# Kernel tuning notes

Measured on AMD Instinct MI355X. Metric: run time of the kernel, lower is better.

## Reference

```python
import jax, jax.numpy as jnp
import numpy as np

KNOTS = 16
BN_EPS = 1e-5  # flax BatchNorm default


def _normalize_spline_params(W, H, D):
    # widths/heights sum to 1 over the [0,1] hypercube; slopes positive
    dx = jax.nn.softmax(W, axis=-1)          # (N, d, K) bin widths
    dy = jax.nn.softmax(H, axis=-1)          # (N, d, K) bin heights
    sl = jax.nn.softplus(D)                  # (N, d, K-1) interior knot slopes
    return dx, dy, sl


def _gather_bin(a, idx):
    # a: (N, d, K'), idx: (N, d) -> (N, d)
    return jnp.take_along_axis(a, idx[..., None], axis=-1)[..., 0]


def _rqs_forward(t, dx, dy, sl):
    """Rational-quadratic spline on [0,1] (Durkan et al. 2019); identity outside.
    t: (N, d); dx, dy: (N, d, K); sl: (N, d, K-1).
    Returns y: (N, d), log_det: (N,)."""
    K = dx.shape[-1]
    zero = jnp.zeros_like(dx[..., :1])
    one = jnp.ones_like(dx[..., :1])
    xk = jnp.concatenate([zero, jnp.cumsum(dx, axis=-1)], axis=-1)   # (N, d, K+1) knot x
    yk = jnp.concatenate([zero, jnp.cumsum(dy, axis=-1)], axis=-1)   # (N, d, K+1) knot y
    dk = jnp.concatenate([one, sl, one], axis=-1)                    # (N, d, K+1) knot slopes

    in_bounds = (t >= 0.0) & (t <= 1.0)
    tc = jnp.clip(t, 0.0, 1.0)
    # per-element bin search (vectorized searchsorted)
    idx = jnp.clip(jnp.sum((tc[..., None] >= xk).astype(jnp.int32), axis=-1) - 1, 0, K - 1)

    xk_b = _gather_bin(xk, idx)
    yk_b = _gather_bin(yk, idx)
    dx_b = _gather_bin(dx, idx)
    dy_b = _gather_bin(dy, idx)
    d0 = _gather_bin(dk, idx)
    d1 = _gather_bin(dk, idx + 1)

    xi = (tc - xk_b) / dx_b            # position within bin, in [0,1]
    s = dy_b / dx_b                    # bin mean slope
    xi1m = xi * (1.0 - xi)
    den = s + (d0 + d1 - 2.0 * s) * xi1m
    y_in = yk_b + dy_b * (s * xi * xi + d0 * xi1m) / den
    dydx = s * s * (d1 * xi * xi + 2.0 * s * xi1m + d0 * (1.0 - xi) ** 2) / (den * den)

    y = jnp.where(in_bounds, y_in, t)
    log_det = jnp.sum(jnp.where(in_bounds, jnp.log(dydx), 0.0), axis=1)  # (N,)
    return y, log_det


def setup_inputs() -> dict:
    key = jax.random.key(0)
    ks = jax.random.split(key, 8)
    N, D, C = 65536, 64, 16
    d = D // 2
    spline_dim = 3 * KNOTS - 1
    cin = d + C           # conditioner input width: hstack(xc, c)
    H1, H2 = 128, 128     # layers=(128,128)

    def dense(k, fi, fo):
        return (jax.random.normal(k, (fi, fo), jnp.float32) / np.float32(np.sqrt(fi)))

    return {
        "x": jax.random.uniform(ks[0], (N, D), jnp.float32),
        "c": jax.random.normal(ks[1], (N, C), jnp.float32),
        "bn_scale": jnp.ones((cin,), jnp.float32),
        "bn_bias": jnp.zeros((cin,), jnp.float32),
        "bn_mean": 0.1 * jax.random.normal(ks[2], (cin,), jnp.float32),
        "bn_var": jax.random.uniform(ks[3], (cin,), jnp.float32, minval=0.5, maxval=1.5),
        "W0": dense(ks[4], cin, H1), "b0": jnp.zeros((H1,), jnp.float32),
        "W1": dense(ks[5], H1, H2), "b1": jnp.zeros((H2,), jnp.float32),
        "W2": dense(ks[6], H2, d * spline_dim), "b2": jnp.zeros((d * spline_dim,), jnp.float32),
    }


def reference(x, c, bn_scale, bn_bias, bn_mean, bn_var, W0, b0, W1, b1, W2, b2):
    N, D = x.shape
    d = D // 2
    xt, xc = x[:, :d], x[:, d:]
    h = jnp.hstack((xc, c))
    # BatchNorm in eval mode (use_running_average=True)
    h = (h - bn_mean) * jax.lax.rsqrt(bn_var + BN_EPS) * bn_scale + bn_bias
    h = jax.nn.swish(h @ W0 + b0)
    h = jax.nn.swish(h @ W1 + b1)
    p = (h @ W2 + b2).reshape(N, d, 3 * KNOTS - 1)
    dx, dy, sl = _normalize_spline_params(
        p[..., :KNOTS], p[..., KNOTS:2 * KNOTS], p[..., 2 * KNOTS:])
    yt, log_det = _rqs_forward(xt, dx, dy, sl)
    y = jnp.hstack((yt, xc))
    return y, log_det
```

## Files before the change

kernel.cpp:

```cpp
#include <hip/hip_runtime.h>
#include <math.h>

#define BN_EPS 1e-5f
#define ROWS 64

typedef __attribute__((ext_vector_type(8))) short short8;
typedef __attribute__((ext_vector_type(4))) float float4v;

__device__ __forceinline__ unsigned short f2bf(float f) {
    union { float f; unsigned int u; } v; v.f = f;
    unsigned int r = v.u + 0x7FFF + ((v.u >> 16) & 1);
    return (unsigned short)(r >> 16);
}
__device__ __forceinline__ float softplus_f(float v) {
    float e = __expf(-fabsf(v));
    float r = __logf(1.f + e);
    return v > 0.f ? v + r : r;
}
__device__ __forceinline__ float swish_f(float a) {
    return a / (1.f + __expf(-a));
}

#define PREP_WIDE_THREADS (1536 * 128 + 128 * 128)
__global__ void prep_weights(const float* __restrict__ W0, const float* __restrict__ W1,
                             const float* __restrict__ W2, const float* __restrict__ b0,
                             const float* __restrict__ b2,
                             const float* __restrict__ bn_scale, const float* __restrict__ bn_bias,
                             const float* __restrict__ bn_mean, const float* __restrict__ bn_var,
                             unsigned short* __restrict__ Wt0, unsigned short* __restrict__ Wt1,
                             unsigned short* __restrict__ Wt2, float* __restrict__ b0p,
                             float* __restrict__ b2p) {
    const int bid = blockIdx.x, tid = threadIdx.x;
    if (bid < 832) {
        int i = bid * 256 + tid;
        if (i < 1536 * 128) {
            int k = i / 1536, colp = i - k * 1536;
            int dd = colp / 48, j = colp - dd * 48;
            float v = (j < 47) ? W2[k * 1504 + dd * 47 + j] : 0.f;
            Wt2[(size_t)colp * 128 + k] = f2bf(v);
        } else {
            int i2 = i - 1536 * 128;
            int k = i2 >> 7, n = i2 & 127;
            Wt1[n * 128 + k] = f2bf(W1[k * 128 + n]);
        }
        return;
    }
    if (bid == 832) {
        __shared__ float lds[48 * 129 + 96];
        float* a   = lds + 48 * 129;
        float* bsh = a + 48;
        if (tid < 48) {
            float av = bn_scale[tid] * rsqrtf(bn_var[tid] + BN_EPS);
            a[tid] = av;
            bsh[tid] = bn_bias[tid] - bn_mean[tid] * av;
        }
        for (int idx = tid; idx < 48 * 128; idx += 256) {
            int k = idx >> 7, n = idx & 127;
            lds[k * 129 + n] = W0[k * 128 + n];
        }
        __syncthreads();
        #pragma unroll 4
        for (int it = 0; it < 32; ++it) {
            int n = (tid >> 6) + it * 4;
            int k = tid & 63;
            float v = (k < 48) ? lds[k * 129 + n] * a[k] : 0.f;
            Wt0[n * 64 + k] = f2bf(v);
        }
        if (tid < 128) {
            float s = b0[tid];
            #pragma unroll
            for (int k = 0; k < 48; ++k) s += bsh[k] * lds[k * 129 + tid];
            b0p[tid] = s;
        }
        return;
    }
    for (int e = tid; e < 32 * 48; e += 256) {
        int dd = e / 48, j = e - dd * 48;
        b2p[e] = (j < 47) ? b2[dd * 47 + j] : 0.f;
    }
}

__launch_bounds__(256, 4)
__global__ void nsc_mfma(const float* __restrict__ x, const float* __restrict__ c,
                         const unsigned short* __restrict__ Wt0, const float* __restrict__ b0p,
                         const unsigned short* __restrict__ Wt1, const float* __restrict__ b1,
                         const unsigned short* __restrict__ Wt2, const float* __restrict__ b2p,
                         float* __restrict__ out, int N) {
    __shared__ __align__(16) char smem[38912];
    unsigned short* h0 = (unsigned short*)smem;
    unsigned short* h2 = (unsigned short*)smem;
    unsigned short* h1 = (unsigned short*)(smem + 17408);
    float*          ldp = (float*)(smem + 17408 + 20480);

    const int tid  = threadIdx.x;
    const int lane = tid & 63;
    const int l    = lane & 15;
    const int q    = lane >> 4;
    const int wu   = __builtin_amdgcn_readfirstlane(tid >> 6);
    const int r0   = blockIdx.x * ROWS;
    float* pw = (float*)(smem + 17408) + wu * (64 * 20);

    for (int idx = tid; idx < 64 * 64; idx += 256) {
        int r = idx >> 6, j = idx & 63;
        float h = 0.f;
        if (j < 48) {
            int row = r0 + r;
            h = (j < 32) ? x[(size_t)row * 64 + 32 + j] : c[(size_t)row * 16 + (j - 32)];
        }
        h0[r * 72 + j] = f2bf(h);
    }
    for (int idx = tid; idx < 64 * 8; idx += 256) {
        int r = idx >> 3, ch = idx & 7;
        float4v v = *(const float4v*)(x + (size_t)(r0 + r) * 64 + 32 + ch * 4);
        *(float4v*)(out + (size_t)(r0 + r) * 64 + 32 + ch * 4) = v;
    }
    __syncthreads();

    {
        float4v acc[2][4];
        float4v z = {0.f, 0.f, 0.f, 0.f};
        #pragma unroll
        for (int nt = 0; nt < 2; ++nt)
            #pragma unroll
            for (int mt = 0; mt < 4; ++mt) acc[nt][mt] = z;
        #pragma unroll
        for (int ks = 0; ks < 2; ++ks) {
            short8 a[4];
            #pragma unroll
            for (int mt = 0; mt < 4; ++mt)
                a[mt] = *(const short8*)(h0 + (mt * 16 + l) * 72 + ks * 32 + (q << 3));
            #pragma unroll
            for (int nt = 0; nt < 2; ++nt) {
                int n0 = (wu * 2 + nt) * 16;
                short8 b = *(const short8*)(Wt0 + (n0 + l) * 64 + ks * 32 + (q << 3));
                #pragma unroll
                for (int mt = 0; mt < 4; ++mt)
                    acc[nt][mt] = __builtin_amdgcn_mfma_f32_16x16x32_bf16(a[mt], b, acc[nt][mt], 0, 0, 0);
            }
        }
        #pragma unroll
        for (int nt = 0; nt < 2; ++nt) {
            int n0 = (wu * 2 + nt) * 16;
            float bb = b0p[n0 + l];
            #pragma unroll
            for (int mt = 0; mt < 4; ++mt)
                #pragma unroll
                for (int r = 0; r < 4; ++r)
                    h1[(mt * 16 + q * 4 + r) * 136 + n0 + l] = f2bf(swish_f(acc[nt][mt][r] + bb));
        }
    }
    __syncthreads();

    {
        float4v acc[2][4];
        float4v z = {0.f, 0.f, 0.f, 0.f};
        #pragma unroll
        for (int nt = 0; nt < 2; ++nt)
            #pragma unroll
            for (int mt = 0; mt < 4; ++mt) acc[nt][mt] = z;
        #pragma unroll
        for (int ks = 0; ks < 4; ++ks) {
            short8 a[4];
            #pragma unroll
            for (int mt = 0; mt < 4; ++mt)
                a[mt] = *(const short8*)(h1 + (mt * 16 + l) * 136 + ks * 32 + (q << 3));
            #pragma unroll
            for (int nt = 0; nt < 2; ++nt) {
                int n0 = (wu * 2 + nt) * 16;
                short8 b = *(const short8*)(Wt1 + (n0 + l) * 128 + ks * 32 + (q << 3));
                #pragma unroll
                for (int mt = 0; mt < 4; ++mt)
                    acc[nt][mt] = __builtin_amdgcn_mfma_f32_16x16x32_bf16(a[mt], b, acc[nt][mt], 0, 0, 0);
            }
        }
        #pragma unroll
        for (int nt = 0; nt < 2; ++nt) {
            int n0 = (wu * 2 + nt) * 16;
            float bb = b1[n0 + l];
            #pragma unroll
            for (int mt = 0; mt < 4; ++mt)
                #pragma unroll
                for (int r = 0; r < 4; ++r)
                    h2[(mt * 16 + q * 4 + r) * 136 + n0 + l] = f2bf(swish_f(acc[nt][mt][r] + bb));
        }
    }
    __syncthreads();

    float ld_local = 0.f;
    float yreg[8];
    for (int pass = 0; pass < 8; ++pass) {
        const int d = wu * 8 + pass;
        float t = x[(size_t)(r0 + lane) * 64 + d];
        bool inb = (t >= 0.f) && (t <= 1.f);
        float tc = fminf(fmaxf(t, 0.f), 1.f);

        float4v acc[3][4];
        float4v z = {0.f, 0.f, 0.f, 0.f};
        #pragma unroll
        for (int jt = 0; jt < 3; ++jt)
            #pragma unroll
            for (int smt = 0; smt < 4; ++smt) acc[jt][smt] = z;
        #pragma unroll
        for (int ks = 0; ks < 4; ++ks) {
            short8 bf[4];
            #pragma unroll
            for (int smt = 0; smt < 4; ++smt)
                bf[smt] = *(const short8*)(h2 + (smt * 16 + l) * 136 + ks * 32 + (q << 3));
            #pragma unroll
            for (int jt = 0; jt < 3; ++jt) {
                short8 a = *(const short8*)(Wt2 + (size_t)(d * 48 + jt * 16 + l) * 128 + ks * 32 + (q << 3));
                #pragma unroll
                for (int smt = 0; smt < 4; ++smt)
                    acc[jt][smt] = __builtin_amdgcn_mfma_f32_16x16x32_bf16(a, bf[smt], acc[jt][smt], 0, 0, 0);
            }
        }

        float pr[16];
        {
            float4v bj = *(const float4v*)(b2p + d * 48 + (q << 2));
            #pragma unroll
            for (int smt = 0; smt < 4; ++smt)
                *(float4v*)(pw + (smt * 16 + l) * 20 + (q << 2)) = acc[0][smt] + bj;
            #pragma unroll
            for (int c2 = 0; c2 < 4; ++c2)
                *(float4v*)(pr + c2 * 4) = *(const float4v*)(pw + lane * 20 + c2 * 4);
        }
        float mW = pr[0];
        #pragma unroll
        for (int i = 1; i < 16; ++i) mW = fmaxf(mW, pr[i]);
        float sW = 0.f;
        #pragma unroll
        for (int i = 0; i < 16; ++i) { pr[i] = __expf(pr[i] - mW); sW += pr[i]; }
        float invW = 1.f / sW;
        float cum = 0.f, xkb = 0.f, dxb = pr[0] * invW;
        int idx = 0;
        #pragma unroll
        for (int i = 0; i < 16; ++i) {
            float dxi = pr[i] * invW;
            bool cnd = (tc >= cum);
            idx = cnd ? i   : idx;
            xkb = cnd ? cum : xkb;
            dxb = cnd ? dxi : dxb;
            cum += dxi;
        }

        {
            float4v bj = *(const float4v*)(b2p + d * 48 + 16 + (q << 2));
            #pragma unroll
            for (int smt = 0; smt < 4; ++smt)
                *(float4v*)(pw + (smt * 16 + l) * 20 + (q << 2)) = acc[1][smt] + bj;
            #pragma unroll
            for (int c2 = 0; c2 < 4; ++c2)
                *(float4v*)(pr + c2 * 4) = *(const float4v*)(pw + lane * 20 + c2 * 4);
        }
        float mH = pr[0];
        #pragma unroll
        for (int i = 1; i < 16; ++i) mH = fmaxf(mH, pr[i]);
        float sH = 0.f;
        #pragma unroll
        for (int i = 0; i < 16; ++i) { pr[i] = __expf(pr[i] - mH); sH += pr[i]; }
        float invH = 1.f / sH;
        float ykb = 0.f, dyb = pr[0] * invH;
        #pragma unroll
        for (int i = 0; i < 16; ++i) {
            float dyi = pr[i] * invH;
            ykb += (i < idx) ? dyi : 0.f;
            dyb  = (i == idx) ? dyi : dyb;
        }

        {
            float4v bj = *(const float4v*)(b2p + d * 48 + 32 + (q << 2));
            #pragma unroll
            for (int smt = 0; smt < 4; ++smt)
                *(float4v*)(pw + (smt * 16 + l) * 20 + (q << 2)) = acc[2][smt] + bj;
        }
        int i0 = (idx > 0)  ? idx - 1 : 0;
        int i1 = (idx < 15) ? idx     : 14;
        float pa0 = pw[lane * 20 + i0];
        float pa1 = pw[lane * 20 + i1];
        float d0 = (idx == 0)  ? 1.f : softplus_f(pa0);
        float d1 = (idx == 15) ? 1.f : softplus_f(pa1);

        float xi  = (tc - xkb) / dxb;
        float s   = dyb / dxb;
        float xim = 1.f - xi;
        float x1m = xi * xim;
        float den = s + (d0 + d1 - 2.f * s) * x1m;
        float y_in = ykb + dyb * (s * xi * xi + d0 * x1m) / den;
        float dydx = s * s * (d1 * xi * xi + 2.f * s * x1m + d0 * xim * xim) / (den * den);

        yreg[pass] = inb ? y_in : t;
        ld_local += inb ? __logf(dydx) : 0.f;
    }

    {
        float4v* o = (float4v*)(out + (size_t)(r0 + lane) * 64 + wu * 8);
        o[0] = *(const float4v*)(yreg);
        o[1] = *(const float4v*)(yreg + 4);
    }
    ldp[wu * 64 + lane] = ld_local;
    __syncthreads();
    if (tid < 64) {
        out[(size_t)N * 64 + r0 + tid] =
            ldp[tid] + ldp[64 + tid] + ldp[128 + tid] + ldp[192 + tid];
    }
}

extern "C" void kernel_launch(void* const* d_in, const int* in_sizes, int n_in,
                              void* d_out, int out_size, void* d_ws, size_t ws_size,
                              hipStream_t stream) {
    const float* x        = (const float*)d_in[0];
    const float* c        = (const float*)d_in[1];
    const float* bn_scale = (const float*)d_in[2];
    const float* bn_bias  = (const float*)d_in[3];
    const float* bn_mean  = (const float*)d_in[4];
    const float* bn_var   = (const float*)d_in[5];
    const float* W0       = (const float*)d_in[6];
    const float* b0       = (const float*)d_in[7];
    const float* W1       = (const float*)d_in[8];
    const float* b1       = (const float*)d_in[9];
    const float* W2       = (const float*)d_in[10];
    const float* b2       = (const float*)d_in[11];
    float* out = (float*)d_out;

    unsigned short* Wt0 = (unsigned short*)d_ws;
    unsigned short* Wt1 = Wt0 + 128 * 64;
    unsigned short* Wt2 = Wt1 + 128 * 128;
    float*          b2p = (float*)(Wt2 + 1536 * 128);
    float*          b0p = b2p + 32 * 48;

    const int N = in_sizes[0] / 64;
    prep_weights<<<834, 256, 0, stream>>>(W0, W1, W2, b0, b2,
                                          bn_scale, bn_bias, bn_mean, bn_var,
                                          Wt0, Wt1, Wt2, b0p, b2p);
    nsc_mfma<<<N / ROWS, 256, 0, stream>>>(x, c, Wt0, b0p, Wt1, b1, Wt2, b2p, out, N);
}
```

Before: 163.4 us.

## Transpose MFMA spline params in registers via permlane swaps instead of LDS

Replaces the per-pass LDS round trip that transposed MFMA accumulator tiles into per-row parameter vectors with v_permlane32/16 swap instructions, so each lane gets its row's 16 values directly in registers. It also drops the LDS scratch (shrinking shared memory), uses tree reductions for max/sum, searches bins on unnormalized cumulative widths scaled by the sum, and replaces divisions with reciprocals. This removes LDS traffic and waits from the epilogue at the cost of extra register pressure and inline asm that depends on gfx950-specific permlane instructions.

```diff
diff --git a/kernel.cpp b/kernel.cpp
--- a/kernel.cpp
+++ b/kernel.cpp
@@ -19,6 +19,26 @@
 }
 __device__ __forceinline__ float swish_f(float a) {
     return a / (1.f + __expf(-a));
+}
+
+#define SWAP32(a, b) asm("v_permlane32_swap_b32 %0, %1" : "+v"(a), "+v"(b));
+#define SWAP16(a, b) asm("v_permlane16_swap_b32 %0, %1" : "+v"(a), "+v"(b));
+
+__device__ __forceinline__ float max16(const float* p) {
+    float a = fmaxf(p[0], p[1]),  b = fmaxf(p[2], p[3]);
+    float c = fmaxf(p[4], p[5]),  d = fmaxf(p[6], p[7]);
+    float e = fmaxf(p[8], p[9]),  f = fmaxf(p[10], p[11]);
+    float g = fmaxf(p[12], p[13]), h = fmaxf(p[14], p[15]);
+    a = fmaxf(a, b); c = fmaxf(c, d); e = fmaxf(e, f); g = fmaxf(g, h);
+    return fmaxf(fmaxf(a, c), fmaxf(e, g));
+}
+__device__ __forceinline__ float sum16(const float* p) {
+    float a = p[0] + p[1],  b = p[2] + p[3];
+    float c = p[4] + p[5],  d = p[6] + p[7];
+    float e = p[8] + p[9],  f = p[10] + p[11];
+    float g = p[12] + p[13], h = p[14] + p[15];
+    a += b; c += d; e += f; g += h;
+    return (a + c) + (e + g);
 }
 
 #define PREP_WIDE_THREADS (1536 * 128 + 128 * 128)
@@ -86,11 +106,11 @@
                          const unsigned short* __restrict__ Wt1, const float* __restrict__ b1,
                          const unsigned short* __restrict__ Wt2, const float* __restrict__ b2p,
                          float* __restrict__ out, int N) {
-    __shared__ __align__(16) char smem[38912];
+    __shared__ __align__(16) char smem[34816];
     unsigned short* h0 = (unsigned short*)smem;
     unsigned short* h2 = (unsigned short*)smem;
     unsigned short* h1 = (unsigned short*)(smem + 17408);
-    float*          ldp = (float*)(smem + 17408 + 20480);
+    float*          ldp = (float*)(smem + 17408);
 
     const int tid  = threadIdx.x;
     const int lane = tid & 63;
@@ -98,7 +118,6 @@
     const int q    = lane >> 4;
     const int wu   = __builtin_amdgcn_readfirstlane(tid >> 6);
     const int r0   = blockIdx.x * ROWS;
-    float* pw = (float*)(smem + 17408) + wu * (64 * 20);
 
     for (int idx = tid; idx < 64 * 64; idx += 256) {
         int r = idx >> 6, j = idx & 63;
@@ -185,6 +204,21 @@
         }
     }
     __syncthreads();
+
+#define TRANSP(JT, BOFF, PR)                                                 \
+    {                                                                        \
+        float4v bj = *(const float4v*)(b2p + d * 48 + (BOFF) + (q << 2));    \
+        _Pragma("unroll")                                                    \
+        for (int r = 0; r < 4; ++r) {                                        \
+            float a0 = acc[JT][0][r] + bj[r];                                \
+            float a1 = acc[JT][1][r] + bj[r];                                \
+            float a2 = acc[JT][2][r] + bj[r];                                \
+            float a3 = acc[JT][3][r] + bj[r];                                \
+            SWAP32(a0, a2) SWAP32(a1, a3)                                    \
+            SWAP16(a0, a1) SWAP16(a2, a3)                                    \
+            PR[r] = a0; PR[4 + r] = a1; PR[8 + r] = a2; PR[12 + r] = a3;     \
+        }                                                                    \
+    }
 
     float ld_local = 0.f;
     float yreg[8];
@@ -215,79 +249,58 @@
             }
         }
 
-        float pr[16];
-        {
-            float4v bj = *(const float4v*)(b2p + d * 48 + (q << 2));
-            #pragma unroll
-            for (int smt = 0; smt < 4; ++smt)
-                *(float4v*)(pw + (smt * 16 + l) * 20 + (q << 2)) = acc[0][smt] + bj;
-            #pragma unroll
-            for (int c2 = 0; c2 < 4; ++c2)
-                *(float4v*)(pr + c2 * 4) = *(const float4v*)(pw + lane * 20 + c2 * 4);
-        }
-        float mW = pr[0];
-        #pragma unroll
-        for (int i = 1; i < 16; ++i) mW = fmaxf(mW, pr[i]);
-        float sW = 0.f;
-        #pragma unroll
-        for (int i = 0; i < 16; ++i) { pr[i] = __expf(pr[i] - mW); sW += pr[i]; }
-        float invW = 1.f / sW;
-        float cum = 0.f, xkb = 0.f, dxb = pr[0] * invW;
+        float prW[16];
+        TRANSP(0, 0, prW)
+        float mW = max16(prW);
+        #pragma unroll
+        for (int i = 0; i < 16; ++i) prW[i] = __expf(prW[i] - mW);
+        float sW = sum16(prW);
+        float ts = tc * sW;
+        float cum = 0.f, xkb = 0.f, dxb = prW[0];
         int idx = 0;
         #pragma unroll
         for (int i = 0; i < 16; ++i) {
-            float dxi = pr[i] * invW;
-            bool cnd = (tc >= cum);
-            idx = cnd ? i   : idx;
+            bool cnd = (ts >= cum);
+            idx = cnd ? i : idx;
             xkb = cnd ? cum : xkb;
-            dxb = cnd ? dxi : dxb;
-            cum += dxi;
-        }
-
-        {
-            float4v bj = *(const float4v*)(b2p + d * 48 + 16 + (q << 2));
-            #pragma unroll
-            for (int smt = 0; smt < 4; ++smt)
-                *(float4v*)(pw + (smt * 16 + l) * 20 + (q << 2)) = acc[1][smt] + bj;
-            #pragma unroll
-            for (int c2 = 0; c2 < 4; ++c2)
-                *(float4v*)(pr + c2 * 4) = *(const float4v*)(pw + lane * 20 + c2 * 4);
-        }
-        float mH = pr[0];
-        #pragma unroll
-        for (int i = 1; i < 16; ++i) mH = fmaxf(mH, pr[i]);
-        float sH = 0.f;
-        #pragma unroll
-        for (int i = 0; i < 16; ++i) { pr[i] = __expf(pr[i] - mH); sH += pr[i]; }
+            dxb = cnd ? prW[i] : dxb;
+            cum += prW[i];
+        }
+
+        float prH[16];
+        TRANSP(1, 16, prH)
+        float mH = max16(prH);
+        #pragma unroll
+        for (int i = 0; i < 16; ++i) prH[i] = __expf(prH[i] - mH);
+        float sH = sum16(prH);
         float invH = 1.f / sH;
-        float ykb = 0.f, dyb = pr[0] * invH;
+
+        float prD[16];
+        TRANSP(2, 32, prD)
+        float ykb = 0.f, dyb = prH[0], pa0 = prD[0], pa1 = prD[0];
         #pragma unroll
         for (int i = 0; i < 16; ++i) {
-            float dyi = pr[i] * invH;
-            ykb += (i < idx) ? dyi : 0.f;
-            dyb  = (i == idx) ? dyi : dyb;
-        }
-
-        {
-            float4v bj = *(const float4v*)(b2p + d * 48 + 32 + (q << 2));
-            #pragma unroll
-            for (int smt = 0; smt < 4; ++smt)
-                *(float4v*)(pw + (smt * 16 + l) * 20 + (q << 2)) = acc[2][smt] + bj;
-        }
-        int i0 = (idx > 0)  ? idx - 1 : 0;
-        int i1 = (idx < 15) ? idx     : 14;
-        float pa0 = pw[lane * 20 + i0];
-        float pa1 = pw[lane * 20 + i1];
+            bool lt = (i < idx);
+            bool eq = (i == idx);
+            ykb += lt ? prH[i] : 0.f;
+            dyb = eq ? prH[i] : dyb;
+            pa0 = eq ? prD[(i > 0) ? (i - 1) : 0] : pa0;
+            pa1 = eq ? prD[i] : pa1;
+        }
         float d0 = (idx == 0)  ? 1.f : softplus_f(pa0);
         float d1 = (idx == 15) ? 1.f : softplus_f(pa1);
 
-        float xi  = (tc - xkb) / dxb;
-        float s   = dyb / dxb;
+        float rdx = 1.f / dxb;
+        float xi  = (ts - xkb) * rdx;
+        float dyn = dyb * invH;
+        float ykn = ykb * invH;
+        float s   = dyn * sW * rdx;
         float xim = 1.f - xi;
         float x1m = xi * xim;
         float den = s + (d0 + d1 - 2.f * s) * x1m;
-        float y_in = ykb + dyb * (s * xi * xi + d0 * x1m) / den;
-        float dydx = s * s * (d1 * xi * xi + 2.f * s * x1m + d0 * xim * xim) / (den * den);
+        float rden = 1.f / den;
+        float y_in = ykn + dyn * (s * xi * xi + d0 * x1m) * rden;
+        float dydx = s * s * (d1 * xi * xi + 2.f * s * x1m + d0 * xim * xim) * (rden * rden);
 
         yreg[pass] = inb ? y_in : t;
         ld_local += inb ? __logf(dydx) : 0.f;
```

After: 200.6 us. 1.23x slower.
